# Performance work log

Measured on AMD Instinct MI355X. Metric: run time of the kernel, lower is better.

## Reference

```python
import jax, jax.numpy as jnp
import numpy as np

D_MODEL = 1024
NUM_HEADS = 16
D_K = D_MODEL // NUM_HEADS
THETA = 10000.0


def apply_rope(x, positions):
    # x: [b, h, s, d_k]; positions: [b, s] int32
    half = D_K // 2
    inv_freq = THETA ** (-jnp.arange(half, dtype=jnp.float32) * 2.0 / D_K)  # [half]
    angles = positions[:, None, :, None].astype(jnp.float32) * inv_freq  # [b,1,s,half]
    cos, sin = jnp.cos(angles), jnp.sin(angles)
    x1 = x[..., 0::2]  # even dims
    x2 = x[..., 1::2]  # odd dims
    out_even = x1 * cos - x2 * sin
    out_odd = x1 * sin + x2 * cos
    # re-interleave
    out = jnp.stack([out_even, out_odd], axis=-1)
    return out.reshape(x.shape)


def setup_inputs() -> dict:
    key = jax.random.key(0)
    ks = jax.random.split(key, 5)
    b, s = 2, 2048
    scale = 0.02
    return {
        "x": jax.random.normal(ks[0], (b, s, D_MODEL), dtype=jnp.float32),
        "Wq": jax.random.normal(ks[1], (D_MODEL, D_MODEL), dtype=jnp.float32) * scale,
        "Wk": jax.random.normal(ks[2], (D_MODEL, D_MODEL), dtype=jnp.float32) * scale,
        "Wv": jax.random.normal(ks[3], (D_MODEL, D_MODEL), dtype=jnp.float32) * scale,
        "Wo": jax.random.normal(ks[4], (D_MODEL, D_MODEL), dtype=jnp.float32) * scale,
    }


def reference(x, Wq, Wk, Wv, Wo):
    b, s, _ = x.shape
    # Linear(d, d) applied as x @ W^T (torch Linear convention, no bias)
    Q = x @ Wq.T
    K = x @ Wk.T
    V = x @ Wv.T
    # split heads: [b, s, h*d] -> [b, h, s, d]
    split = lambda t: t.reshape(b, s, NUM_HEADS, D_K).transpose(0, 2, 1, 3)
    Q, K, V = split(Q), split(K), split(V)
    positions = jnp.broadcast_to(jnp.arange(s, dtype=jnp.int32), (b, s))
    Q = apply_rope(Q, positions)
    K = apply_rope(K, positions)
    scores = jnp.einsum('bhqd,bhkd->bhqk', Q, K) / jnp.sqrt(jnp.float32(D_K))
    causal = jnp.tril(jnp.ones((s, s), dtype=bool))
    scores = jnp.where(causal[None, None], scores, -jnp.inf)
    attn = jax.nn.softmax(scores, axis=-1)
    out = jnp.einsum('bhqk,bhkd->bhqd', attn, V)
    out = out.transpose(0, 2, 1, 3).reshape(b, s, D_MODEL)
    return out @ Wo.T
```

## Files before the change

### kernel.cpp

```cpp
#include <hip/hip_runtime.h>

typedef __attribute__((ext_vector_type(8))) short bf16x8;
typedef __attribute__((ext_vector_type(4))) float f32x4;
typedef __attribute__((ext_vector_type(16))) float f32x16;

typedef const __attribute__((address_space(1))) unsigned int gu32;
typedef __attribute__((address_space(3))) unsigned int lu32;

__device__ __forceinline__ void async16(const void* g, void* l) {
  __builtin_amdgcn_global_load_lds((gu32*)g, (lu32*)l, 16, 0, 0);
}

__device__ __forceinline__ unsigned short f2bf(float f) {
  unsigned int u = __float_as_uint(f);
  u += 0x7fffu + ((u >> 16) & 1u);
  return (unsigned short)(u >> 16);
}
__device__ __forceinline__ float b2f(unsigned short s) {
  return __uint_as_float(((unsigned int)s) << 16);
}
__device__ __forceinline__ unsigned int cvtpk(float lo, float hi) {
  unsigned int w;
  asm("v_cvt_pk_bf16_f32 %0, %1, %2" : "=v"(w) : "v"(lo), "v"(hi));
  return w;
}
__device__ __forceinline__ void plswap(unsigned int& x, unsigned int& y) {
  asm("v_permlane32_swap_b32 %0, %1" : "+v"(x), "+v"(y));
}
__device__ __forceinline__ float max3f(float a, float b, float c) {
  float d;
  asm("v_max3_f32 %0, %1, %2, %3" : "=v"(d) : "v"(a), "v"(b), "v"(c));
  return d;
}

__global__ __launch_bounds__(256) void cvt_k(const float* __restrict__ in,
                                             unsigned short* __restrict__ out,
                                             int n4) {
  int i = blockIdx.x * 256 + threadIdx.x;
  if (i >= n4) return;
  float4 v = ((const float4*)in)[i];
  ushort4 o;
  o.x = f2bf(v.x); o.y = f2bf(v.y); o.z = f2bf(v.z); o.w = f2bf(v.w);
  ((ushort4*)out)[i] = o;
}

template <int WRITE_F32>
__global__ __launch_bounds__(256) void gemm_bt(const unsigned short* __restrict__ A,
                                               const unsigned short* __restrict__ B,
                                               void* __restrict__ Cp, int N, int K) {
  __shared__ __align__(16) unsigned short Al[2][128 * 32];
  __shared__ __align__(16) unsigned short Bl[2][128 * 32];
  const int t = threadIdx.x;
  const int w = t >> 6, l = t & 63;
  const int wm = w >> 1, wn = w & 1;
  const int lr = l & 15, lg = l >> 4;
  const long bm = (long)blockIdx.x * 128, bn = (long)blockIdx.y * 128;
  const int srow = t >> 2;
  const int c8 = t & 3;
  const int KT = K >> 5;
  f32x4 acc[4][4] = {};

  auto STAGE = [&](int ts) {
    const int bi = ts & 1;
    const int k0 = ts * 32;
    #pragma unroll
    for (int r = 0; r < 2; ++r) {
      int row = r * 64 + srow;
      async16(&A[(bm + row) * (long)K + k0 + c8 * 8], &Al[bi][row * 32 + c8 * 8]);
      async16(&B[(bn + row) * (long)K + k0 + c8 * 8], &Bl[bi][row * 32 + c8 * 8]);
    }
  };

  STAGE(0);
  for (int kt = 0; kt < KT; ++kt) {
    const int cur = kt & 1;
    asm volatile("s_waitcnt vmcnt(0)" ::: "memory");
    __builtin_amdgcn_s_barrier();
    __builtin_amdgcn_sched_barrier(0);
    if (kt + 1 < KT) STAGE(kt + 1);
    bf16x8 af[4], bf[4];
    #pragma unroll
    for (int i = 0; i < 4; ++i) {
      af[i] = *(const bf16x8*)&Al[cur][(wm * 64 + i * 16 + lr) * 32 + lg * 8];
      bf[i] = *(const bf16x8*)&Bl[cur][(wn * 64 + i * 16 + lr) * 32 + lg * 8];
    }
    #pragma unroll
    for (int i = 0; i < 4; ++i)
      #pragma unroll
      for (int j = 0; j < 4; ++j)
        acc[i][j] = __builtin_amdgcn_mfma_f32_16x16x32_bf16(af[i], bf[j], acc[i][j], 0, 0, 0);
  }
  #pragma unroll
  for (int i = 0; i < 4; ++i)
    #pragma unroll
    for (int j = 0; j < 4; ++j)
      #pragma unroll
      for (int r = 0; r < 4; ++r) {
        long row = bm + wm * 64 + i * 16 + lg * 4 + r;
        long col = bn + wn * 64 + j * 16 + lr;
        float v = acc[i][j][r];
        if (WRITE_F32) ((float*)Cp)[row * N + col] = v;
        else ((unsigned short*)Cp)[row * N + col] = f2bf(v);
      }
}

__global__ __launch_bounds__(256) void rope_k(unsigned short* __restrict__ QKV) {
  __shared__ float csl[32], snl[32];
  const int row = blockIdx.x;
  const int s = row & 2047;
  const int t = threadIdx.x;
  if (t < 32) {
    float invf = exp2f((float)t * (-13.287712379549449f / 32.0f));
    float sn, cs;
    sincosf((float)s * invf, &sn, &cs);
    csl[t] = cs; snl[t] = sn;
  }
  __syncthreads();
  const int col0 = (t < 128) ? t * 8 : 1024 + (t - 128) * 8;
  const int i0 = (t & 7) * 4;
  unsigned short* p = &QKV[(size_t)row * 3072 + col0];
  bf16x8 v = *(const bf16x8*)p;
  bf16x8 o;
  #pragma unroll
  for (int j = 0; j < 4; ++j) {
    float x1 = b2f((unsigned short)v[2 * j]);
    float x2 = b2f((unsigned short)v[2 * j + 1]);
    float cs = csl[i0 + j], sn = snl[i0 + j];
    o[2 * j]     = (short)f2bf(x1 * cs - x2 * sn);
    o[2 * j + 1] = (short)f2bf(x1 * sn + x2 * cs);
  }
  *(bf16x8*)p = o;
}

__global__ __launch_bounds__(256) void vtr_k(const unsigned short* __restrict__ QKV,
                                             unsigned short* __restrict__ Vt) {
  __shared__ unsigned short tl[64][66];
  const int kt = blockIdx.x;
  const int bh = blockIdx.y;
  const int b = bh >> 4, h = bh & 15;
  const int t = threadIdx.x;
  const int row = t >> 3, c8 = t & 7;
  #pragma unroll
  for (int r = 0; r < 2; ++r) {
    int k = r * 32 + row;
    bf16x8 v = *(const bf16x8*)&QKV[((long)b * 2048 + kt * 64 + k) * 3072 + 2048 + h * 64 + c8 * 8];
    #pragma unroll
    for (int j = 0; j < 8; ++j) tl[c8 * 8 + j][k] = (unsigned short)v[j];
  }
  __syncthreads();
  #pragma unroll
  for (int r = 0; r < 2; ++r) {
    int d = r * 32 + row;
    ushort4 a, bq;
    a.x = tl[d][c8 * 8 + 0]; a.y = tl[d][c8 * 8 + 1];
    a.z = tl[d][c8 * 8 + 2]; a.w = tl[d][c8 * 8 + 3];
    bq.x = tl[d][c8 * 8 + 4]; bq.y = tl[d][c8 * 8 + 5];
    bq.z = tl[d][c8 * 8 + 6]; bq.w = tl[d][c8 * 8 + 7];
    long off = ((long)bh * 64 + d) * 2048 + kt * 64 + c8 * 8;
    *(ushort4*)&Vt[off] = a;
    *(ushort4*)&Vt[off + 4] = bq;
  }
}

__global__ __launch_bounds__(256) void attn_k(const unsigned short* __restrict__ QKV,
                                              const unsigned short* __restrict__ VtG,
                                              unsigned short* __restrict__ O) {
  __shared__ __align__(16) unsigned short Kl[3][64 * 64];
  __shared__ __align__(16) unsigned short Vl[3][64 * 64];
  const int t = threadIdx.x;
  const int w = t >> 6, l = t & 63;
  const int q31 = l & 31, hi = l >> 5;
  const int bh = blockIdx.x;
  const int y = (int)blockIdx.y;
  const int qt = (y < 8) ? (15 - y) : (y - 8);
  const int b = bh >> 4, h = bh & 15;
  const int Qb = qt * 128;
  const long rowb = (long)b * 2048;
  const int L = 3072;
  const int NT = 2 * qt + 2;
  const float cexp = 0.125f * 1.4426950408889634f;

  const int qmy = Qb + 32 * w + q31;
  const long qgrow = rowb + qmy;
  const int ktmax = (Qb + 32 * w) >> 6;

  bf16x8 qf[4];
  #pragma unroll
  for (int dk = 0; dk < 4; ++dk)
    qf[dk] = *(const bf16x8*)&QKV[qgrow * L + h * 64 + dk * 16 + hi * 8];

  bf16x8 onesf;
  #pragma unroll
  for (int j = 0; j < 8; ++j) onesf[j] = (short)0x3F80;

  float m_ = -1e30f;
  f32x16 oa[2], la;
  #pragma unroll
  for (int r = 0; r < 16; ++r) { oa[0][r] = 0.0f; oa[1][r] = 0.0f; la[r] = 0.0f; }

  auto STAGE = [&](int ts) {
    const int bi = ts % 3;
    const long kb = rowb + (long)ts * 64;
    const long vrowb = (long)bh * 64;
    #pragma unroll
    for (int r = 0; r < 2; ++r) {
      int row = w * 16 + r * 8 + (l >> 3);
      int c8s = ((l & 7) ^ (row & 7)) * 8;
      async16(&QKV[(kb + row) * L + 1024 + h * 64 + c8s], &Kl[bi][row * 64 + (l & 7) * 8]);
      async16(&VtG[(vrowb + row) * 2048 + ts * 64 + c8s], &Vl[bi][row * 64 + (l & 7) * 8]);
    }
  };

  auto QK = [&](f32x16 (&st)[2], int bi) {
    #pragma unroll
    for (int kt2 = 0; kt2 < 2; ++kt2)
      #pragma unroll
      for (int r = 0; r < 16; ++r) st[kt2][r] = 0.0f;
    __builtin_amdgcn_s_setprio(1);
    #pragma unroll
    for (int dk = 0; dk < 4; ++dk)
      #pragma unroll
      for (int kt2 = 0; kt2 < 2; ++kt2) {
        int krow = kt2 * 32 + q31;
        bf16x8 kfr = *(const bf16x8*)&Kl[bi][krow * 64 + (((2 * dk + hi) ^ (krow & 7)) * 8)];
        st[kt2] = __builtin_amdgcn_mfma_f32_32x32x16_bf16(kfr, qf[dk], st[kt2], 0, 0, 0);
      }
    __builtin_amdgcn_s_setprio(0);
  };

  auto SMPV = [&](f32x16 (&st)[2], int kt) {
    if (kt == ktmax) {
      #pragma unroll
      for (int kt2 = 0; kt2 < 2; ++kt2)
        #pragma unroll
        for (int r = 0; r < 16; ++r) {
          int kg = kt * 64 + kt2 * 32 + (r & 3) + 8 * (r >> 2) + 4 * hi;
          if (kg > qmy) st[kt2][r] = -1e30f;
        }
    }
    float m0[8];
    #pragma unroll
    for (int i = 0; i < 8; ++i)
      m0[i] = max3f(st[0][i], st[0][i + 8], fmaxf(st[1][i], st[1][i + 8]));
    float mt = max3f(max3f(m0[0], m0[1], m0[2]), max3f(m0[3], m0[4], m0[5]),
                     fmaxf(m0[6], m0[7]));
    if (__any((mt - m_) * cexp > 8.0f)) {
      float mg = fmaxf(mt, __shfl_xor(mt, 32, 64));
      float mn = fmaxf(m_, mg);
      float al = __builtin_amdgcn_exp2f((m_ - mn) * cexp);
      m_ = mn;
      la[0] *= al;
      #pragma unroll
      for (int dt = 0; dt < 2; ++dt)
        #pragma unroll
        for (int r = 0; r < 16; ++r) oa[dt][r] *= al;
    }
    const float mc = m_ * cexp;
    #pragma unroll
    for (int kt2 = 0; kt2 < 2; ++kt2)
      #pragma unroll
      for (int r = 0; r < 16; ++r)
        st[kt2][r] = __builtin_amdgcn_exp2f(fmaf(st[kt2][r], cexp, -mc));
    bf16x8 pfr[4];
    #pragma unroll
    for (int ks = 0; ks < 4; ++ks) {
      int tt = ks >> 1, gX = 2 * (ks & 1), gY = gX + 1;
      unsigned int x1 = cvtpk(st[tt][4 * gX + 0], st[tt][4 * gX + 1]);
      unsigned int y1 = cvtpk(st[tt][4 * gY + 0], st[tt][4 * gY + 1]);
      plswap(x1, y1);
      unsigned int x2 = cvtpk(st[tt][4 * gX + 2], st[tt][4 * gX + 3]);
      unsigned int y2 = cvtpk(st[tt][4 * gY + 2], st[tt][4 * gY + 3]);
      plswap(x2, y2);
      union { unsigned int u[4]; bf16x8 b; } cc;
      cc.u[0] = x1; cc.u[1] = x2; cc.u[2] = y1; cc.u[3] = y2;
      pfr[ks] = cc.b;
    }
    const int vb = kt % 3;
    __builtin_amdgcn_s_setprio(1);
    #pragma unroll
    for (int ks = 0; ks < 4; ++ks) {
      la = __builtin_amdgcn_mfma_f32_32x32x16_bf16(onesf, pfr[ks], la, 0, 0, 0);
      #pragma unroll
      for (int dt = 0; dt < 2; ++dt) {
        int vrow = dt * 32 + q31;
        bf16x8 vf = *(const bf16x8*)&Vl[vb][vrow * 64 + (((2 * ks + hi) ^ (vrow & 7)) * 8)];
        oa[dt] = __builtin_amdgcn_mfma_f32_32x32x16_bf16(vf, pfr[ks], oa[dt], 0, 0, 0);
      }
    }
    __builtin_amdgcn_s_setprio(0);
  };

  f32x16 stA[2], stB[2];

  STAGE(0);
  STAGE(1);
  asm volatile("s_waitcnt vmcnt(4)" ::: "memory");
  __builtin_amdgcn_s_barrier();
  __builtin_amdgcn_sched_barrier(0);
  QK(stA, 0);

  auto STEP = [&](f32x16 (&cur)[2], f32x16 (&nxt)[2], int kt) {
    asm volatile("s_waitcnt vmcnt(0)" ::: "memory");
    __builtin_amdgcn_s_barrier();
    __builtin_amdgcn_sched_barrier(0);
    if (kt + 1 < NT && kt + 1 <= ktmax) QK(nxt, (kt + 1) % 3);
    if (kt + 2 < NT) STAGE(kt + 2);
    if (kt <= ktmax) SMPV(cur, kt);
  };

  int kt = 0;
  while (kt < NT) {
    STEP(stA, stB, kt); ++kt;
    if (kt < NT) { STEP(stB, stA, kt); ++kt; }
  }

  float inv = 1.0f / la[0];
  #pragma unroll
  for (int dt = 0; dt < 2; ++dt)
    #pragma unroll
    for (int g = 0; g < 4; ++g) {
      ushort4 o4;
      o4.x = f2bf(oa[dt][4 * g + 0] * inv);
      o4.y = f2bf(oa[dt][4 * g + 1] * inv);
      o4.z = f2bf(oa[dt][4 * g + 2] * inv);
      o4.w = f2bf(oa[dt][4 * g + 3] * inv);
      *(ushort4*)&O[qgrow * 1024 + h * 64 + dt * 32 + 8 * g + 4 * hi] = o4;
    }
}

extern "C" void kernel_launch(void* const* d_in, const int* in_sizes, int n_in,
                              void* d_out, int out_size, void* d_ws, size_t ws_size,
                              hipStream_t stream) {
  const float* x  = (const float*)d_in[0];
  const float* Wq = (const float*)d_in[1];
  const float* Wk = (const float*)d_in[2];
  const float* Wv = (const float*)d_in[3];
  const float* Wo = (const float*)d_in[4];
  char* ws = (char*)d_ws;
  unsigned short* xb   = (unsigned short*)(ws);
  unsigned short* Wb   = (unsigned short*)(ws + (8u << 20));
  unsigned short* Wob  = (unsigned short*)(ws + (14u << 20));
  unsigned short* QKVb = (unsigned short*)(ws + (16u << 20));
  unsigned short* Ob   = (unsigned short*)(ws + (40u << 20));
  unsigned short* Vtg  = xb;

  cvt_k<<<4096, 256, 0, stream>>>(x, xb, 4096 * 1024 / 4);
  cvt_k<<<1024, 256, 0, stream>>>(Wq, Wb, 1024 * 1024 / 4);
  cvt_k<<<1024, 256, 0, stream>>>(Wk, Wb + 1024 * 1024, 1024 * 1024 / 4);
  cvt_k<<<1024, 256, 0, stream>>>(Wv, Wb + 2 * 1024 * 1024, 1024 * 1024 / 4);
  cvt_k<<<1024, 256, 0, stream>>>(Wo, Wob, 1024 * 1024 / 4);

  gemm_bt<0><<<dim3(32, 24), 256, 0, stream>>>(xb, Wb, QKVb, 3072, 1024);
  rope_k<<<4096, 256, 0, stream>>>(QKVb);
  vtr_k<<<dim3(32, 32), 256, 0, stream>>>(QKVb, Vtg);
  attn_k<<<dim3(32, 16), 256, 0, stream>>>(QKVb, Vtg, Ob);
  gemm_bt<1><<<dim3(32, 8), 256, 0, stream>>>(Ob, Wob, d_out, 1024, 1024);
}
```

Baseline: 130.4 us.

## Split long causal attention tiles across two blocks with a combine pass

The seven longest query tiles (qt 9..15) are now split into two key-range chunks, each handled by its own block. Each chunk writes unnormalized fp32 partial outputs plus its running max and sum to scratch, reusing d_out and the Wq-Wk bf16 region, which are dead by then. A new combine kernel merges the two partials into bf16 output. This balances the causal triangle's uneven work over more blocks (23 per head instead of 16), at the cost of an extra launch and fp32 partial traffic. The four weight conversions are also merged into one launch.

Measured after the change: 142.3 us. 1.09x slower.

```diff
diff --git a/kernel.cpp b/kernel.cpp
--- a/kernel.cpp
+++ b/kernel.cpp
@@ -42,6 +42,24 @@
   ushort4 o;
   o.x = f2bf(v.x); o.y = f2bf(v.y); o.z = f2bf(v.z); o.w = f2bf(v.w);
   ((ushort4*)out)[i] = o;
+}
+
+__global__ __launch_bounds__(256) void cvtw_k(const float* __restrict__ Wq,
+                                              const float* __restrict__ Wk,
+                                              const float* __restrict__ Wv,
+                                              const float* __restrict__ Wo,
+                                              unsigned short* __restrict__ Wb,
+                                              unsigned short* __restrict__ Wob) {
+  int i = blockIdx.x * 256 + threadIdx.x;
+  int wsel = i >> 18;
+  int j = i & 0x3FFFF;
+  const float* src = (wsel == 0) ? Wq : (wsel == 1) ? Wk : (wsel == 2) ? Wv : Wo;
+  unsigned short* dst = (wsel == 0) ? Wb : (wsel == 1) ? Wb + (1 << 20)
+                       : (wsel == 2) ? Wb + (2 << 20) : Wob;
+  float4 v = ((const float4*)src)[j];
+  ushort4 o;
+  o.x = f2bf(v.x); o.y = f2bf(v.y); o.z = f2bf(v.z); o.w = f2bf(v.w);
+  ((ushort4*)dst)[j] = o;
 }
 
 template <int WRITE_F32>
@@ -162,9 +180,14 @@
   }
 }
 
+__constant__ int qtA[23] = {8,15,15,7,14,14,13,13,6,12,12,11,11,5,10,10,9,9,4,3,2,1,0};
+__constant__ int chA[23] = {-1,0,1,-1,0,1,0,1,-1,0,1,0,1,-1,0,1,0,1,-1,-1,-1,-1,-1};
+
 __global__ __launch_bounds__(256) void attn_k(const unsigned short* __restrict__ QKV,
                                               const unsigned short* __restrict__ VtG,
-                                              unsigned short* __restrict__ O) {
+                                              unsigned short* __restrict__ O,
+                                              float* __restrict__ Opart,
+                                              float* __restrict__ MLb) {
   __shared__ __align__(16) unsigned short Kl[3][64 * 64];
   __shared__ __align__(16) unsigned short Vl[3][64 * 64];
   const int t = threadIdx.x;
@@ -172,12 +195,13 @@
   const int q31 = l & 31, hi = l >> 5;
   const int bh = blockIdx.x;
   const int y = (int)blockIdx.y;
-  const int qt = (y < 8) ? (15 - y) : (y - 8);
+  const int qt = qtA[y], ch = chA[y];
   const int b = bh >> 4, h = bh & 15;
   const int Qb = qt * 128;
   const long rowb = (long)b * 2048;
   const int L = 3072;
-  const int NT = 2 * qt + 2;
+  const int KT0 = (ch == 1) ? (qt + 1) : 0;
+  const int KT1 = (ch == 0) ? (qt + 1) : (2 * qt + 2);
   const float cexp = 0.125f * 1.4426950408889634f;
 
   const int qmy = Qb + 32 * w + q31;
@@ -292,40 +316,90 @@
 
   f32x16 stA[2], stB[2];
 
-  STAGE(0);
-  STAGE(1);
+  STAGE(KT0);
+  STAGE(KT0 + 1);
   asm volatile("s_waitcnt vmcnt(4)" ::: "memory");
   __builtin_amdgcn_s_barrier();
   __builtin_amdgcn_sched_barrier(0);
-  QK(stA, 0);
+  QK(stA, KT0 % 3);
 
   auto STEP = [&](f32x16 (&cur)[2], f32x16 (&nxt)[2], int kt) {
     asm volatile("s_waitcnt vmcnt(0)" ::: "memory");
     __builtin_amdgcn_s_barrier();
     __builtin_amdgcn_sched_barrier(0);
-    if (kt + 1 < NT && kt + 1 <= ktmax) QK(nxt, (kt + 1) % 3);
-    if (kt + 2 < NT) STAGE(kt + 2);
+    if (kt + 1 < KT1 && kt + 1 <= ktmax) QK(nxt, (kt + 1) % 3);
+    if (kt + 2 < KT1) STAGE(kt + 2);
     if (kt <= ktmax) SMPV(cur, kt);
   };
 
-  int kt = 0;
-  while (kt < NT) {
+  int kt = KT0;
+  while (kt < KT1) {
     STEP(stA, stB, kt); ++kt;
-    if (kt < NT) { STEP(stB, stA, kt); ++kt; }
-  }
-
-  float inv = 1.0f / la[0];
-  #pragma unroll
-  for (int dt = 0; dt < 2; ++dt)
-    #pragma unroll
-    for (int g = 0; g < 4; ++g) {
-      ushort4 o4;
-      o4.x = f2bf(oa[dt][4 * g + 0] * inv);
-      o4.y = f2bf(oa[dt][4 * g + 1] * inv);
-      o4.z = f2bf(oa[dt][4 * g + 2] * inv);
-      o4.w = f2bf(oa[dt][4 * g + 3] * inv);
-      *(ushort4*)&O[qgrow * 1024 + h * 64 + dt * 32 + 8 * g + 4 * hi] = o4;
-    }
+    if (kt < KT1) { STEP(stB, stA, kt); ++kt; }
+  }
+
+  const int rit = 32 * w + q31;
+  if (ch < 0) {
+    float inv = 1.0f / la[0];
+    #pragma unroll
+    for (int dt = 0; dt < 2; ++dt)
+      #pragma unroll
+      for (int g = 0; g < 4; ++g) {
+        ushort4 o4;
+        o4.x = f2bf(oa[dt][4 * g + 0] * inv);
+        o4.y = f2bf(oa[dt][4 * g + 1] * inv);
+        o4.z = f2bf(oa[dt][4 * g + 2] * inv);
+        o4.w = f2bf(oa[dt][4 * g + 3] * inv);
+        *(ushort4*)&O[qgrow * 1024 + h * 64 + dt * 32 + 8 * g + 4 * hi] = o4;
+      }
+  } else {
+    const int p = bh * 7 + (qt - 9);
+    float* Op = Opart + (size_t)(p * 2 + ch) * 8192;
+    #pragma unroll
+    for (int dt = 0; dt < 2; ++dt)
+      #pragma unroll
+      for (int g = 0; g < 4; ++g) {
+        float4 o4;
+        o4.x = oa[dt][4 * g + 0]; o4.y = oa[dt][4 * g + 1];
+        o4.z = oa[dt][4 * g + 2]; o4.w = oa[dt][4 * g + 3];
+        *(float4*)&Op[rit * 64 + dt * 32 + 8 * g + 4 * hi] = o4;
+      }
+    MLb[(size_t)(p * 2 + ch) * 256 + rit * 2 + 0] = m_;
+    MLb[(size_t)(p * 2 + ch) * 256 + rit * 2 + 1] = la[0];
+  }
+}
+
+__global__ __launch_bounds__(256) void comb_k(const float* __restrict__ Opart,
+                                              const float* __restrict__ MLb,
+                                              unsigned short* __restrict__ O) {
+  const int p = blockIdx.x;
+  const int bh = p / 7, qt = 9 + p % 7;
+  const int b = bh >> 4, h = bh & 15;
+  const int t = threadIdx.x;
+  const int row = t >> 1, half = t & 1;
+  const float cexp = 0.125f * 1.4426950408889634f;
+  float m0 = MLb[(size_t)(p * 2 + 0) * 256 + row * 2 + 0];
+  float l0 = MLb[(size_t)(p * 2 + 0) * 256 + row * 2 + 1];
+  float m1 = MLb[(size_t)(p * 2 + 1) * 256 + row * 2 + 0];
+  float l1 = MLb[(size_t)(p * 2 + 1) * 256 + row * 2 + 1];
+  float M = fmaxf(m0, m1);
+  float e0 = exp2f((m0 - M) * cexp), e1 = exp2f((m1 - M) * cexp);
+  float inv = 1.0f / (e0 * l0 + e1 * l1);
+  const float* O0 = Opart + (size_t)(p * 2 + 0) * 8192 + row * 64 + half * 32;
+  const float* O1 = Opart + (size_t)(p * 2 + 1) * 8192 + row * 64 + half * 32;
+  long orow = (long)b * 2048 + qt * 128 + row;
+  unsigned short* Oo = O + orow * 1024 + h * 64 + half * 32;
+  #pragma unroll
+  for (int j = 0; j < 32; j += 4) {
+    float4 a = *(const float4*)&O0[j];
+    float4 c = *(const float4*)&O1[j];
+    ushort4 o4;
+    o4.x = f2bf((e0 * a.x + e1 * c.x) * inv);
+    o4.y = f2bf((e0 * a.y + e1 * c.y) * inv);
+    o4.z = f2bf((e0 * a.z + e1 * c.z) * inv);
+    o4.w = f2bf((e0 * a.w + e1 * c.w) * inv);
+    *(ushort4*)&Oo[j] = o4;
+  }
 }
 
 extern "C" void kernel_launch(void* const* d_in, const int* in_sizes, int n_in,
@@ -343,16 +417,16 @@
   unsigned short* QKVb = (unsigned short*)(ws + (16u << 20));
   unsigned short* Ob   = (unsigned short*)(ws + (40u << 20));
   unsigned short* Vtg  = xb;
+  float* Opart = (float*)d_out;
+  float* MLbuf = (float*)Wb;
 
   cvt_k<<<4096, 256, 0, stream>>>(x, xb, 4096 * 1024 / 4);
-  cvt_k<<<1024, 256, 0, stream>>>(Wq, Wb, 1024 * 1024 / 4);
-  cvt_k<<<1024, 256, 0, stream>>>(Wk, Wb + 1024 * 1024, 1024 * 1024 / 4);
-  cvt_k<<<1024, 256, 0, stream>>>(Wv, Wb + 2 * 1024 * 1024, 1024 * 1024 / 4);
-  cvt_k<<<1024, 256, 0, stream>>>(Wo, Wob, 1024 * 1024 / 4);
+  cvtw_k<<<4096, 256, 0, stream>>>(Wq, Wk, Wv, Wo, Wb, Wob);
 
   gemm_bt<0><<<dim3(32, 24), 256, 0, stream>>>(xb, Wb, QKVb, 3072, 1024);
   rope_k<<<4096, 256, 0, stream>>>(QKVb);
   vtr_k<<<dim3(32, 32), 256, 0, stream>>>(QKVb, Vtg);
-  attn_k<<<dim3(32, 16), 256, 0, stream>>>(QKVb, Vtg, Ob);
+  attn_k<<<dim3(32, 23), 256, 0, stream>>>(QKVb, Vtg, Ob, Opart, MLbuf);
+  comb_k<<<224, 256, 0, stream>>>(Opart, MLbuf, Ob);
   gemm_bt<1><<<dim3(32, 8), 256, 0, stream>>>(Ob, Wob, d_out, 1024, 1024);
 }
```

## Triple-buffer GEMM LDS staging and merge weight conversions into one launch

Applied to the files above, without the earlier changes.

The GEMM moves from double to triple buffering in LDS, keeping two K-tiles of async global-to-LDS loads in flight and waiting only for the older one (vmcnt(4)) before each barrier. This is meant to hide global load latency. It raises LDS use per block from 32KB to 48KB, which could lower occupancy. Separately, the four weight conversion launches are merged into a single kernel to cut launch overhead.

Result: no change. 128.2 us (-1.7%).

```diff
diff --git a/kernel.cpp b/kernel.cpp
--- a/kernel.cpp
+++ b/kernel.cpp
@@ -44,12 +44,30 @@
   ((ushort4*)out)[i] = o;
 }
 
+__global__ __launch_bounds__(256) void cvtw_k(const float* __restrict__ Wq,
+                                              const float* __restrict__ Wk,
+                                              const float* __restrict__ Wv,
+                                              const float* __restrict__ Wo,
+                                              unsigned short* __restrict__ Wb,
+                                              unsigned short* __restrict__ Wob) {
+  int i = blockIdx.x * 256 + threadIdx.x;
+  int wsel = i >> 18;
+  int j = i & 0x3FFFF;
+  const float* src = (wsel == 0) ? Wq : (wsel == 1) ? Wk : (wsel == 2) ? Wv : Wo;
+  unsigned short* dst = (wsel == 0) ? Wb : (wsel == 1) ? Wb + (1 << 20)
+                       : (wsel == 2) ? Wb + (2 << 20) : Wob;
+  float4 v = ((const float4*)src)[j];
+  ushort4 o;
+  o.x = f2bf(v.x); o.y = f2bf(v.y); o.z = f2bf(v.z); o.w = f2bf(v.w);
+  ((ushort4*)dst)[j] = o;
+}
+
 template <int WRITE_F32>
 __global__ __launch_bounds__(256) void gemm_bt(const unsigned short* __restrict__ A,
                                                const unsigned short* __restrict__ B,
                                                void* __restrict__ Cp, int N, int K) {
-  __shared__ __align__(16) unsigned short Al[2][128 * 32];
-  __shared__ __align__(16) unsigned short Bl[2][128 * 32];
+  __shared__ __align__(16) unsigned short Al[3][128 * 32];
+  __shared__ __align__(16) unsigned short Bl[3][128 * 32];
   const int t = threadIdx.x;
   const int w = t >> 6, l = t & 63;
   const int wm = w >> 1, wn = w & 1;
@@ -61,7 +79,7 @@
   f32x4 acc[4][4] = {};
 
   auto STAGE = [&](int ts) {
-    const int bi = ts & 1;
+    const int bi = ts % 3;
     const int k0 = ts * 32;
     #pragma unroll
     for (int r = 0; r < 2; ++r) {
@@ -72,12 +90,14 @@
   };
 
   STAGE(0);
+  STAGE(1);
   for (int kt = 0; kt < KT; ++kt) {
-    const int cur = kt & 1;
-    asm volatile("s_waitcnt vmcnt(0)" ::: "memory");
+    const int cur = kt % 3;
+    if (kt < KT - 1) asm volatile("s_waitcnt vmcnt(4)" ::: "memory");
+    else             asm volatile("s_waitcnt vmcnt(0)" ::: "memory");
     __builtin_amdgcn_s_barrier();
     __builtin_amdgcn_sched_barrier(0);
-    if (kt + 1 < KT) STAGE(kt + 1);
+    if (kt + 2 < KT) STAGE(kt + 2);
     bf16x8 af[4], bf[4];
     #pragma unroll
     for (int i = 0; i < 4; ++i) {
@@ -345,10 +365,7 @@
   unsigned short* Vtg  = xb;
 
   cvt_k<<<4096, 256, 0, stream>>>(x, xb, 4096 * 1024 / 4);
-  cvt_k<<<1024, 256, 0, stream>>>(Wq, Wb, 1024 * 1024 / 4);
-  cvt_k<<<1024, 256, 0, stream>>>(Wk, Wb + 1024 * 1024, 1024 * 1024 / 4);
-  cvt_k<<<1024, 256, 0, stream>>>(Wv, Wb + 2 * 1024 * 1024, 1024 * 1024 / 4);
-  cvt_k<<<1024, 256, 0, stream>>>(Wo, Wob, 1024 * 1024 / 4);
+  cvtw_k<<<4096, 256, 0, stream>>>(Wq, Wk, Wv, Wo, Wb, Wob);
 
   gemm_bt<0><<<dim3(32, 24), 256, 0, stream>>>(xb, Wb, QKVb, 3072, 1024);
   rope_k<<<4096, 256, 0, stream>>>(QKVb);
```
